# Kernel optimization log

Measured on AMD Instinct MI355X. Metric: run time of the kernel, lower is better.

## Reference

```python
import jax, jax.numpy as jnp
import numpy as np

N_VARS = 50000   # number of variables (graph nodes)
N_TX = 200000    # number of transforms in the bucket (edges)
D = 32           # per-variable slice size (layout.sizes[v])


def setup_inputs() -> dict:
    key = jax.random.key(0)
    k1, k2, k3, k4, k5 = jax.random.split(key, 5)
    theta = jax.random.normal(k1, (N_VARS * D,), dtype=jnp.float32)  # flat variable buffer
    # stacked_params of one TransformBucket: per-transform Linear(D, D)
    W = jax.random.normal(k2, (N_TX, D, D), dtype=jnp.float32) / np.sqrt(D)
    b = jax.random.normal(k3, (N_TX, D), dtype=jnp.float32)
    src_ids = jax.random.randint(k4, (N_TX,), 0, N_VARS)  # gather_indices rows (var id -> slice)
    tgt_ids = jax.random.randint(k5, (N_TX,), 0, N_VARS)  # scatter_indices rows
    return {"theta": theta, "W": W, "b": b, "src_ids": src_ids, "tgt_ids": tgt_ids}


def reference(theta, W, b, src_ids, tgt_ids):
    # Flat buffer viewed as [n_vars, D]; each variable slice is contiguous per Layout.
    tv = theta.reshape(N_VARS, D)
    # Bucketized gather: pull src slices for every transform in the bucket. [E, D]
    x = tv[src_ids]
    # vmapped transform application (stacked Linear params). [E, D]
    preds_e = jnp.einsum("eij,ej->ei", W, x) + b
    # Scatter-reduce predictions back into shared flat layout. [n_vars, D]
    preds = jnp.zeros_like(tv).at[tgt_ids].add(preds_e)
    # Energy residual per variable slice (gaussian energy: 0.5*||theta - pred||^2).
    resid = tv - preds
    return resid.reshape(-1)
```

## Files before the change

### kernel.cpp

```cpp
#include <hip/hip_runtime.h>

#define N_VARS 50000
#define N_TX   200000
#define DSZ    32

#define NWAVES 4000
#define CHUNK  50

typedef float f32x4 __attribute__((ext_vector_type(4)));

__global__ void copy_theta_kernel(const float4* __restrict__ theta,
                                  float4* __restrict__ out, int n4) {
    int i = blockIdx.x * blockDim.x + threadIdx.x;
    int stride = gridDim.x * blockDim.x;
    for (; i < n4; i += stride) out[i] = theta[i];
}

__global__ __launch_bounds__(256)
void transform_scatter_kernel(const float* __restrict__ theta,
                              const float* __restrict__ W,
                              const float* __restrict__ bia,
                              const int* __restrict__ src,
                              const int* __restrict__ tgt,
                              float* __restrict__ out) {
    const int lane = threadIdx.x & 63;
    const int wave = (blockIdx.x * blockDim.x + threadIdx.x) >> 6;

    const int e0 = wave * CHUNK;
    const int e1 = e0 + CHUNK;

    const int j0    = (lane & 7) << 2;
    const int g     = lane >> 3;
    const bool wr   = (lane & 7) < 4;
    const int myIt  = lane & 3;
    const int myRow = myIt * 8 + g;

    for (int e = e0; e < e1; e += 2) {
        const int sA = src[e],     tA = tgt[e];
        const int sB = src[e + 1], tB = tgt[e + 1];

        const f32x4 xA = *reinterpret_cast<const f32x4*>(theta + (size_t)sA * DSZ + j0);
        const f32x4 xB = *reinterpret_cast<const f32x4*>(theta + (size_t)sB * DSZ + j0);

        const f32x4* WA = reinterpret_cast<const f32x4*>(W + (size_t)e * (DSZ * DSZ));
        const f32x4* WB = WA + 256;

        const f32x4 a0 = __builtin_nontemporal_load(WA +   0 + lane);
        const f32x4 a1 = __builtin_nontemporal_load(WA +  64 + lane);
        const f32x4 a2 = __builtin_nontemporal_load(WA + 128 + lane);
        const f32x4 a3 = __builtin_nontemporal_load(WA + 192 + lane);
        const f32x4 c0 = __builtin_nontemporal_load(WB +   0 + lane);
        const f32x4 c1 = __builtin_nontemporal_load(WB +  64 + lane);
        const f32x4 c2 = __builtin_nontemporal_load(WB + 128 + lane);
        const f32x4 c3 = __builtin_nontemporal_load(WB + 192 + lane);

        const float biasA = bia[(size_t)e * DSZ + myRow];
        const float biasB = bia[(size_t)(e + 1) * DSZ + myRow];

        float pA0 = a0.x * xA.x + a0.y * xA.y + a0.z * xA.z + a0.w * xA.w;
        float pA1 = a1.x * xA.x + a1.y * xA.y + a1.z * xA.z + a1.w * xA.w;
        float pA2 = a2.x * xA.x + a2.y * xA.y + a2.z * xA.z + a2.w * xA.w;
        float pA3 = a3.x * xA.x + a3.y * xA.y + a3.z * xA.z + a3.w * xA.w;
        float pB0 = c0.x * xB.x + c0.y * xB.y + c0.z * xB.z + c0.w * xB.w;
        float pB1 = c1.x * xB.x + c1.y * xB.y + c1.z * xB.z + c1.w * xB.w;
        float pB2 = c2.x * xB.x + c2.y * xB.y + c2.z * xB.z + c2.w * xB.w;
        float pB3 = c3.x * xB.x + c3.y * xB.y + c3.z * xB.z + c3.w * xB.w;

        #pragma unroll
        for (int m = 1; m <= 4; m <<= 1) {
            pA0 += __shfl_xor(pA0, m); pA1 += __shfl_xor(pA1, m);
            pA2 += __shfl_xor(pA2, m); pA3 += __shfl_xor(pA3, m);
            pB0 += __shfl_xor(pB0, m); pB1 += __shfl_xor(pB1, m);
            pB2 += __shfl_xor(pB2, m); pB3 += __shfl_xor(pB3, m);
        }

        if (wr) {
            const float vA = (myIt == 0) ? pA0 : (myIt == 1) ? pA1 : (myIt == 2) ? pA2 : pA3;
            const float vB = (myIt == 0) ? pB0 : (myIt == 1) ? pB1 : (myIt == 2) ? pB2 : pB3;
            atomicAdd(out + (size_t)tA * DSZ + myRow, -(vA + biasA));
            atomicAdd(out + (size_t)tB * DSZ + myRow, -(vB + biasB));
        }
    }
}

extern "C" void kernel_launch(void* const* d_in, const int* in_sizes, int n_in,
                              void* d_out, int out_size, void* d_ws, size_t ws_size,
                              hipStream_t stream) {
    const float* theta = (const float*)d_in[0];
    const float* W     = (const float*)d_in[1];
    const float* b     = (const float*)d_in[2];
    const int*   src   = (const int*)d_in[3];
    const int*   tgt   = (const int*)d_in[4];
    float* out = (float*)d_out;

    const int n4 = (N_VARS * DSZ) / 4;
    copy_theta_kernel<<<1024, 256, 0, stream>>>((const float4*)theta, (float4*)out, n4);

    const int blocks = NWAVES / 4;
    transform_scatter_kernel<<<blocks, 256, 0, stream>>>(theta, W, b, src, tgt, out);
}
```

Baseline: 159.7 us.

## Fuse theta copy into scatter kernel via atomic add after memset

Replaces the separate theta copy kernel with a memset of the output followed by one fused kernel. Each thread atomically adds theta into the output, then waves in 1000 blocks of 200 edges each process edge pairs. Bias loads become nontemporal. This removes one kernel launch and the copy pass, but turns the theta copy into 1.6M scalar atomics plus a memset, and the grid is reshaped.

```diff
diff --git a/kernel.cpp b/kernel.cpp
--- a/kernel.cpp
+++ b/kernel.cpp
@@ -4,30 +4,28 @@
 #define N_TX   200000
 #define DSZ    32
 
-#define NWAVES 4000
-#define CHUNK  50
+#define EDGES_PER_BLOCK 200
+#define NBLOCKS (N_TX / EDGES_PER_BLOCK)
 
 typedef float f32x4 __attribute__((ext_vector_type(4)));
 
-__global__ void copy_theta_kernel(const float4* __restrict__ theta,
-                                  float4* __restrict__ out, int n4) {
-    int i = blockIdx.x * blockDim.x + threadIdx.x;
-    int stride = gridDim.x * blockDim.x;
-    for (; i < n4; i += stride) out[i] = theta[i];
-}
+__global__ __launch_bounds__(256)
+void fused_transform_kernel(const float* __restrict__ theta,
+                            const float* __restrict__ W,
+                            const float* __restrict__ bia,
+                            const int* __restrict__ src,
+                            const int* __restrict__ tgt,
+                            float* __restrict__ out) {
+    const int lane = threadIdx.x & 63;
+    const int w    = threadIdx.x >> 6;
+    const int base = blockIdx.x * EDGES_PER_BLOCK;
 
-__global__ __launch_bounds__(256)
-void transform_scatter_kernel(const float* __restrict__ theta,
-                              const float* __restrict__ W,
-                              const float* __restrict__ bia,
-                              const int* __restrict__ src,
-                              const int* __restrict__ tgt,
-                              float* __restrict__ out) {
-    const int lane = threadIdx.x & 63;
-    const int wave = (blockIdx.x * blockDim.x + threadIdx.x) >> 6;
-
-    const int e0 = wave * CHUNK;
-    const int e1 = e0 + CHUNK;
+    {
+        const int n = N_VARS * DSZ;
+        const int stride = gridDim.x * blockDim.x;
+        for (int i = blockIdx.x * blockDim.x + threadIdx.x; i < n; i += stride)
+            atomicAdd(out + i, theta[i]);
+    }
 
     const int j0    = (lane & 7) << 2;
     const int g     = lane >> 3;
@@ -35,7 +33,9 @@
     const int myIt  = lane & 3;
     const int myRow = myIt * 8 + g;
 
-    for (int e = e0; e < e1; e += 2) {
+    for (int p = w; p < EDGES_PER_BLOCK / 2; p += 4) {
+        const int e = base + 2 * p;
+
         const int sA = src[e],     tA = tgt[e];
         const int sB = src[e + 1], tB = tgt[e + 1];
 
@@ -54,8 +54,8 @@
         const f32x4 c2 = __builtin_nontemporal_load(WB + 128 + lane);
         const f32x4 c3 = __builtin_nontemporal_load(WB + 192 + lane);
 
-        const float biasA = bia[(size_t)e * DSZ + myRow];
-        const float biasB = bia[(size_t)(e + 1) * DSZ + myRow];
+        const float biasA = __builtin_nontemporal_load(bia + (size_t)e * DSZ + myRow);
+        const float biasB = __builtin_nontemporal_load(bia + (size_t)(e + 1) * DSZ + myRow);
 
         float pA0 = a0.x * xA.x + a0.y * xA.y + a0.z * xA.z + a0.w * xA.w;
         float pA1 = a1.x * xA.x + a1.y * xA.y + a1.z * xA.z + a1.w * xA.w;
@@ -93,9 +93,7 @@
     const int*   tgt   = (const int*)d_in[4];
     float* out = (float*)d_out;
 
-    const int n4 = (N_VARS * DSZ) / 4;
-    copy_theta_kernel<<<1024, 256, 0, stream>>>((const float4*)theta, (float4*)out, n4);
+    hipMemsetAsync(out, 0, (size_t)N_VARS * DSZ * sizeof(float), stream);
 
-    const int blocks = NWAVES / 4;
-    transform_scatter_kernel<<<blocks, 256, 0, stream>>>(theta, W, b, src, tgt, out);
+    fused_transform_kernel<<<NBLOCKS, 256, 0, stream>>>(theta, W, b, src, tgt, out);
 }
```

Measured after the change: 166.7 us. +4.4%, slower.

## Interleave edge pairs across waves, prefetch indices, issue atomics from all lanes

Applied to the files above, without the earlier changes.

Each wave now takes pairs in a strided pattern (pair p, p+NWAVES, ...) instead of a contiguous chunk, so at any moment the waves together read a contiguous region of W. The next iteration's src/tgt indices are loaded before the current compute, hiding the index-load latency in front of the dependent theta gather. The atomics are merged into one instruction in which every lane is active: half the lanes write for edge A and half for edge B, replacing two half-masked atomic instructions. Bias is now read with a nontemporal load. The loop is kept rolled, and the final iteration prefetches a dummy index that is never used.

```diff
diff --git a/kernel.cpp b/kernel.cpp
--- a/kernel.cpp
+++ b/kernel.cpp
@@ -5,7 +5,8 @@
 #define DSZ    32
 
 #define NWAVES 4000
-#define CHUNK  50
+#define NPAIRS (N_TX / 2)
+#define PAIRS_PER_WAVE (NPAIRS / NWAVES)
 
 typedef float f32x4 __attribute__((ext_vector_type(4)));
 
@@ -26,18 +27,18 @@
     const int lane = threadIdx.x & 63;
     const int wave = (blockIdx.x * blockDim.x + threadIdx.x) >> 6;
 
-    const int e0 = wave * CHUNK;
-    const int e1 = e0 + CHUNK;
+    const int j0     = (lane & 7) << 2;
+    const int g      = lane >> 3;
+    const int myRow  = (lane & 3) * 8 + g;
+    const bool hiB   = (lane & 4) != 0;
 
-    const int j0    = (lane & 7) << 2;
-    const int g     = lane >> 3;
-    const bool wr   = (lane & 7) < 4;
-    const int myIt  = lane & 3;
-    const int myRow = myIt * 8 + g;
+    int p  = wave;
+    int sA = src[2 * p], sB = src[2 * p + 1];
+    int tA = tgt[2 * p], tB = tgt[2 * p + 1];
 
-    for (int e = e0; e < e1; e += 2) {
-        const int sA = src[e],     tA = tgt[e];
-        const int sB = src[e + 1], tB = tgt[e + 1];
+    #pragma unroll 1
+    for (int it = 0; it < PAIRS_PER_WAVE; ++it) {
+        const int e = 2 * p;
 
         const f32x4 xA = *reinterpret_cast<const f32x4*>(theta + (size_t)sA * DSZ + j0);
         const f32x4 xB = *reinterpret_cast<const f32x4*>(theta + (size_t)sB * DSZ + j0);
@@ -54,8 +55,13 @@
         const f32x4 c2 = __builtin_nontemporal_load(WB + 128 + lane);
         const f32x4 c3 = __builtin_nontemporal_load(WB + 192 + lane);
 
-        const float biasA = bia[(size_t)e * DSZ + myRow];
-        const float biasB = bia[(size_t)(e + 1) * DSZ + myRow];
+        const float biasv =
+            __builtin_nontemporal_load(bia + ((size_t)e + (hiB ? 1 : 0)) * DSZ + myRow);
+
+        const int pn = p + NWAVES;
+        const int pc = (it + 1 < PAIRS_PER_WAVE) ? pn : wave;
+        const int sA2 = src[2 * pc], sB2 = src[2 * pc + 1];
+        const int tA2 = tgt[2 * pc], tB2 = tgt[2 * pc + 1];
 
         float pA0 = a0.x * xA.x + a0.y * xA.y + a0.z * xA.z + a0.w * xA.w;
         float pA1 = a1.x * xA.x + a1.y * xA.y + a1.z * xA.z + a1.w * xA.w;
@@ -74,12 +80,15 @@
             pB2 += __shfl_xor(pB2, m); pB3 += __shfl_xor(pB3, m);
         }
 
-        if (wr) {
-            const float vA = (myIt == 0) ? pA0 : (myIt == 1) ? pA1 : (myIt == 2) ? pA2 : pA3;
-            const float vB = (myIt == 0) ? pB0 : (myIt == 1) ? pB1 : (myIt == 2) ? pB2 : pB3;
-            atomicAdd(out + (size_t)tA * DSZ + myRow, -(vA + biasA));
-            atomicAdd(out + (size_t)tB * DSZ + myRow, -(vB + biasB));
-        }
+        const int   r   = lane & 3;
+        const float sA_ = (r == 0) ? pA0 : (r == 1) ? pA1 : (r == 2) ? pA2 : pA3;
+        const float sB_ = (r == 0) ? pB0 : (r == 1) ? pB1 : (r == 2) ? pB2 : pB3;
+        const float val = hiB ? sB_ : sA_;
+        const int   te  = hiB ? tB : tA;
+
+        atomicAdd(out + (size_t)te * DSZ + myRow, -(val + biasv));
+
+        p = pn; sA = sA2; sB = sB2; tA = tA2; tB = tB2;
     }
 }
 
@@ -96,6 +105,5 @@
     const int n4 = (N_VARS * DSZ) / 4;
     copy_theta_kernel<<<1024, 256, 0, stream>>>((const float4*)theta, (float4*)out, n4);
 
-    const int blocks = NWAVES / 4;
-    transform_scatter_kernel<<<blocks, 256, 0, stream>>>(theta, W, b, src, tgt, out);
+    transform_scatter_kernel<<<NWAVES / 4, 256, 0, stream>>>(theta, W, b, src, tgt, out);
 }
```

After: 155.5 us. 2.6% less time.
